# Kernel optimization log

Hardware: AMD Instinct MI355X
Metric: run time of the kernel (lower is better)

## Reference

```python
import jax, jax.numpy as jnp
import numpy as np

N_HEADS = 8
HEAD_DIM = 64


def setup_inputs() -> dict:
    key = jax.random.key(0)
    ks = jax.random.split(key, 5)
    B, L, D = 2, 2048, 512
    Dh = N_HEADS * HEAD_DIM  # 512
    scale_init = 0.02
    return {
        "x": jax.random.normal(ks[0], (B, L, D), dtype=jnp.float32),
        "wq": jax.random.normal(ks[1], (D, Dh), dtype=jnp.float32) * scale_init,
        "wk": jax.random.normal(ks[2], (D, Dh), dtype=jnp.float32) * scale_init,
        "wv": jax.random.normal(ks[3], (D, Dh), dtype=jnp.float32) * scale_init,
        "wo": jax.random.normal(ks[4], (Dh, D), dtype=jnp.float32) * scale_init,
    }


def reference(x, wq, wk, wv, wo):
    B, L, D = x.shape
    H, Dh = N_HEADS, HEAD_DIM
    scale = 1.0 / (Dh ** 0.5)

    q = (x @ wq).reshape(B, L, H, Dh)
    k = (x @ wk).reshape(B, L, H, Dh)
    v = (x @ wv).reshape(B, L, H, Dh)

    # [B, H, L, S] scores; diagonal (token attending to itself) is masked out.
    scores = jnp.einsum('blhe,bshe->bhls', q, k) * scale
    diag = jnp.eye(L, dtype=bool)  # [L, L]
    scores = jnp.where(diag, -jnp.inf, scores)
    attn = jax.nn.softmax(scores, axis=-1)

    out = jnp.einsum('bhls,bshd->blhd', attn, v).reshape(B, L, H * Dh)
    return out @ wo
```

## Files before the change

### kernel.cpp

```cpp
#include <hip/hip_runtime.h>
#include <hip/hip_bf16.h>
#include <math.h>

typedef __bf16 bf16;
typedef __bf16 bf16x8 __attribute__((ext_vector_type(8)));
typedef float f32x4 __attribute__((ext_vector_type(4)));
typedef unsigned int uint32x4 __attribute__((ext_vector_type(4)));

#define AS1 __attribute__((address_space(1)))
#define AS3 __attribute__((address_space(3)))

__device__ __forceinline__ void gload_lds16(const void* g, void* l) {
  __builtin_amdgcn_global_load_lds((const AS1 void*)g, (AS3 void*)l, 16, 0, 0);
}

__device__ __forceinline__ unsigned packbf16(float a, float b) {
  bf16 x = (bf16)a, y = (bf16)b;
  unsigned short ux, uy;
  __builtin_memcpy(&ux, &x, 2);
  __builtin_memcpy(&uy, &y, 2);
  return (unsigned)ux | ((unsigned)uy << 16);
}

__global__ __launch_bounds__(256) void cvt_x_kernel(const float* __restrict__ x,
                                                    bf16* __restrict__ xb) {
  int i = (blockIdx.x * 256 + threadIdx.x) * 8;
  float4 a = *(const float4*)(x + i);
  float4 b = *(const float4*)(x + i + 4);
  bf16x8 o;
  o[0] = (bf16)a.x; o[1] = (bf16)a.y; o[2] = (bf16)a.z; o[3] = (bf16)a.w;
  o[4] = (bf16)b.x; o[5] = (bf16)b.y; o[6] = (bf16)b.z; o[7] = (bf16)b.w;
  *(bf16x8*)(xb + i) = o;
}

__global__ __launch_bounds__(256) void transpose_w_kernel(
    const float* __restrict__ wq, const float* __restrict__ wk,
    const float* __restrict__ wv, const float* __restrict__ wo,
    bf16* __restrict__ wqkv_t, bf16* __restrict__ wo_t) {
  __shared__ float t[64 * 65];
  int ct = blockIdx.x & 31, kt = blockIdx.x >> 5;
  int p = ct >> 3;
  const float* src = (p == 0) ? wq : (p == 1) ? wk : (p == 2) ? wv : wo;
  int c0 = (ct & 7) * 64;
  int k0 = kt * 64;
  int tid = threadIdx.x;
  for (int i = 0; i < 16; ++i) {
    int idx = i * 256 + tid;
    int r = idx >> 6, c = idx & 63;
    t[r * 65 + c] = src[(size_t)(k0 + r) * 512 + c0 + c];
  }
  __syncthreads();
  for (int i = 0; i < 16; ++i) {
    int idx = i * 256 + tid;
    int cc = idx >> 6, kk = idx & 63;
    float v = t[kk * 65 + cc];
    int col = c0 + cc;
    if (p < 3) wqkv_t[(size_t)(p * 512 + col) * 512 + k0 + kk] = (bf16)v;
    else       wo_t[(size_t)col * 512 + k0 + kk] = (bf16)v;
  }
}

template <int MODE, int BM, int BN>
__global__ __launch_bounds__(256) void gemm_kernel(
    const bf16* __restrict__ A, const bf16* __restrict__ Bt,
    float* __restrict__ Cf, bf16* __restrict__ qw, bf16* __restrict__ kw,
    bf16* __restrict__ vtw, int M, int N, int K) {
  __shared__ bf16 ldsA[BM * 64];
  __shared__ bf16 ldsB[BN * 64];
  constexpr int MF = BM / 32;
  constexpr int NF = BN / 32;
  int tid = threadIdx.x;
  int wave = tid >> 6, l = tid & 63;
  int lr = l & 15, lg = l >> 4;
  int nbm = M / BM;
  int bm = blockIdx.x % nbm, bn = blockIdx.x / nbm;
  int wr = wave >> 1, wc = wave & 1;

  f32x4 acc[MF][NF] = {};

  for (int k0 = 0; k0 < K; k0 += 64) {
    #pragma unroll
    for (int i = 0; i < BM * 128 / 4096; ++i) {
      int off = i * 4096 + tid * 16;
      int r = off >> 7, cb = off & 127;
      gload_lds16((const char*)(A + (size_t)(bm * BM + r) * K + k0) + cb,
                  (char*)ldsA + i * 4096 + wave * 1024);
    }
    #pragma unroll
    for (int i = 0; i < BN * 128 / 4096; ++i) {
      int off = i * 4096 + tid * 16;
      int r = off >> 7, cb = off & 127;
      gload_lds16((const char*)(Bt + (size_t)(bn * BN + r) * K + k0) + cb,
                  (char*)ldsB + i * 4096 + wave * 1024);
    }
    __syncthreads();
    #pragma unroll
    for (int ks = 0; ks < 2; ++ks) {
      bf16x8 af[MF], bfr[NF];
      #pragma unroll
      for (int m = 0; m < MF; ++m)
        af[m] = *(const bf16x8*)(ldsA + (wr * (BM / 2) + m * 16 + lr) * 64 + ks * 32 + lg * 8);
      #pragma unroll
      for (int n = 0; n < NF; ++n)
        bfr[n] = *(const bf16x8*)(ldsB + (wc * (BN / 2) + n * 16 + lr) * 64 + ks * 32 + lg * 8);
      #pragma unroll
      for (int m = 0; m < MF; ++m)
        #pragma unroll
        for (int n = 0; n < NF; ++n)
          acc[m][n] = __builtin_amdgcn_mfma_f32_16x16x32_bf16(af[m], bfr[n], acc[m][n], 0, 0, 0);
    }
    __syncthreads();
  }

  #pragma unroll
  for (int m = 0; m < MF; ++m)
    #pragma unroll
    for (int n = 0; n < NF; ++n)
      #pragma unroll
      for (int j = 0; j < 4; ++j) {
        float v = acc[m][n][j];
        int row = bm * BM + wr * (BM / 2) + m * 16 + lg * 4 + j;
        int col = bn * BN + wc * (BN / 2) + n * 16 + lr;
        if (MODE == 1) {
          Cf[(size_t)row * N + col] = v;
        } else {
          int part = col >> 9, cp = col & 511;
          int h = cp >> 6, d = cp & 63;
          int b = row >> 11, lq = row & 2047;
          size_t bh = (size_t)(b * 8 + h);
          if (part == 0)      qw[(bh * 2048 + lq) * 64 + d] = (bf16)(v * 0.18033688f);
          else if (part == 1) kw[(bh * 2048 + lq) * 64 + d] = (bf16)v;
          else                vtw[(bh * 64 + d) * 2048 + lq] = (bf16)v;
        }
      }
}

__global__ __launch_bounds__(512, 4) void attn_kernel(
    const bf16* __restrict__ qw, const bf16* __restrict__ kw,
    const bf16* __restrict__ vtw,
    bf16* __restrict__ pO0, bf16* __restrict__ pO1,
    bf16* __restrict__ pO2, bf16* __restrict__ pO3,
    float* __restrict__ pL0, float* __restrict__ pL1,
    float* __restrict__ pL2, float* __restrict__ pL3) {
  __shared__ bf16 ldsK[2][64 * 64];
  __shared__ bf16 ldsV[2][64 * 64];

  int swzb = ((blockIdx.x & 7) << 6) | (blockIdx.x >> 3);
  int bh = swzb >> 5, qblk = (swzb >> 2) & 7, kv = swzb & 3;

  int tid = threadIdx.x, wave = tid >> 6, l = tid & 63;
  int lr = l & 15, lg = l >> 4;
  const bf16* Q  = qw  + (size_t)bh * 2048 * 64;
  const bf16* Kp = kw  + (size_t)bh * 2048 * 64;
  const bf16* Vt = vtw + (size_t)bh * 64 * 2048;
  int qbase = qblk * 256 + wave * 32;
  int td = qblk * 4 + (wave >> 1);
  int qoff = (wave & 1) * 32;

  bf16x8 qf[2][2];
  #pragma unroll
  for (int s = 0; s < 2; ++s)
    #pragma unroll
    for (int ks = 0; ks < 2; ++ks)
      qf[s][ks] = *(const bf16x8*)(Q + (size_t)(qbase + s * 16 + lr) * 64 + ks * 32 + lg * 8);

  int rowT = tid >> 3;
  int colT = (tid & 7) * 16;
  int swc = colT ^ ((((rowT & 3) | (((rowT >> 3) & 1) << 2))) << 4);

  int kxor = (((lr & 3) | (((lr >> 2) & 1) << 2)) << 4);
  int vxor = (((lr & 3) | (((lr >> 3) & 1) << 2)) << 4);

  f32x4 acc[2][4] = {};
  float lsum[2] = {0.f, 0.f};

  auto stage = [&](int buf, int t) {
    gload_lds16((const char*)Kp + (size_t)t * 8192 + rowT * 128 + swc,
                (char*)ldsK[buf] + wave * 1024);
    gload_lds16((const char*)Vt + (size_t)t * 128 + (size_t)rowT * 4096 + swc,
                (char*)ldsV[buf] + wave * 1024);
  };

  int t0 = kv * 8;
  stage(0, t0);

  for (int tt = 0; tt < 8; ++tt) {
    int t = t0 + tt;
    int buf = tt & 1;
    if (tt < 7) {
      stage(buf ^ 1, t + 1);
      asm volatile("s_waitcnt vmcnt(2)" ::: "memory");
    } else {
      asm volatile("s_waitcnt vmcnt(0)" ::: "memory");
    }
    __builtin_amdgcn_s_barrier();
    __builtin_amdgcn_sched_barrier(0);

    f32x4 ps[2][4] = {};
    __builtin_amdgcn_s_setprio(1);
    #pragma unroll
    for (int ks = 0; ks < 2; ++ks)
      #pragma unroll
      for (int n = 0; n < 4; ++n) {
        int mrow = ((n >> 1) << 5) + ((lr >> 2) << 3) + ((n & 1) << 2) + (lr & 3);
        bf16x8 kf = *(const bf16x8*)((const char*)ldsK[buf] + mrow * 128 +
                                     ((ks * 64 + lg * 16) ^ kxor));
        #pragma unroll
        for (int s = 0; s < 2; ++s)
          ps[s][n] = __builtin_amdgcn_mfma_f32_16x16x32_bf16(kf, qf[s][ks], ps[s][n], 0, 0, 0);
      }
    __builtin_amdgcn_s_setprio(0);

    if (t == td) {
      #pragma unroll
      for (int s = 0; s < 2; ++s)
        #pragma unroll
        for (int n = 0; n < 4; ++n)
          #pragma unroll
          for (int j = 0; j < 4; ++j)
            if (((n >> 1) * 32 + lg * 8 + (n & 1) * 4 + j) == qoff + s * 16 + lr)
              ps[s][n][j] = -INFINITY;
    }

    bf16x8 pf[2][2];
    #pragma unroll
    for (int s = 0; s < 2; ++s) {
      unsigned u[4][2];
      #pragma unroll
      for (int n = 0; n < 4; ++n) {
        float p0 = __builtin_amdgcn_exp2f(ps[s][n][0]);
        float p1 = __builtin_amdgcn_exp2f(ps[s][n][1]);
        float p2 = __builtin_amdgcn_exp2f(ps[s][n][2]);
        float p3 = __builtin_amdgcn_exp2f(ps[s][n][3]);
        lsum[s] += (p0 + p1) + (p2 + p3);
        u[n][0] = packbf16(p0, p1);
        u[n][1] = packbf16(p2, p3);
      }
      uint32x4 w0 = {u[0][0], u[0][1], u[1][0], u[1][1]};
      uint32x4 w1 = {u[2][0], u[2][1], u[3][0], u[3][1]};
      pf[s][0] = __builtin_bit_cast(bf16x8, w0);
      pf[s][1] = __builtin_bit_cast(bf16x8, w1);
    }

    __builtin_amdgcn_s_setprio(1);
    #pragma unroll
    for (int ks = 0; ks < 2; ++ks)
      #pragma unroll
      for (int n = 0; n < 4; ++n) {
        int vrow = n * 16 + lr;
        bf16x8 vf = *(const bf16x8*)((const char*)ldsV[buf] + vrow * 128 +
                                     ((ks * 64 + lg * 16) ^ vxor));
        #pragma unroll
        for (int s = 0; s < 2; ++s)
          acc[s][n] = __builtin_amdgcn_mfma_f32_16x16x32_bf16(pf[s][ks], vf, acc[s][n], 0, 0, 0);
      }
    __builtin_amdgcn_s_setprio(0);
    __builtin_amdgcn_s_barrier();
  }

  #pragma unroll
  for (int s = 0; s < 2; ++s) {
    lsum[s] += __shfl_xor(lsum[s], 16);
    lsum[s] += __shfl_xor(lsum[s], 32);
  }

  bf16*  pO = (kv == 0) ? pO0 : (kv == 1) ? pO1 : (kv == 2) ? pO2 : pO3;
  float* pL = (kv == 0) ? pL0 : (kv == 1) ? pL1 : (kv == 2) ? pL2 : pL3;
  #pragma unroll
  for (int s = 0; s < 2; ++s) {
    if (lg == 0) pL[(size_t)bh * 2048 + qbase + s * 16 + lr] = lsum[s];
    #pragma unroll
    for (int j = 0; j < 4; ++j) {
      int gq = qbase + s * 16 + lg * 4 + j;
      #pragma unroll
      for (int n = 0; n < 4; ++n)
        pO[((size_t)bh * 2048 + gq) * 64 + n * 16 + lr] = (bf16)acc[s][n][j];
    }
  }
}

__global__ __launch_bounds__(256) void combine_kernel(
    const bf16* __restrict__ pO0, const bf16* __restrict__ pO1,
    const bf16* __restrict__ pO2, const bf16* __restrict__ pO3,
    const float* __restrict__ pL0, const float* __restrict__ pL1,
    const float* __restrict__ pL2, const float* __restrict__ pL3,
    bf16* __restrict__ ao) {
  int idx = blockIdx.x * 256 + threadIdx.x;
  int e8 = idx * 8;
  int row = e8 >> 9, col = e8 & 511;
  int b = row >> 11, lq = row & 2047, h = col >> 6, d0 = col & 63;
  size_t bhq = (size_t)(b * 8 + h) * 2048 + lq;
  size_t src = bhq * 64 + d0;
  bf16x8 v0 = *(const bf16x8*)(pO0 + src);
  bf16x8 v1 = *(const bf16x8*)(pO1 + src);
  bf16x8 v2 = *(const bf16x8*)(pO2 + src);
  bf16x8 v3 = *(const bf16x8*)(pO3 + src);
  float inv = 1.f / (pL0[bhq] + pL1[bhq] + pL2[bhq] + pL3[bhq]);
  bf16x8 o;
  #pragma unroll
  for (int i = 0; i < 8; ++i)
    o[i] = (bf16)(((float)v0[i] + (float)v1[i] + (float)v2[i] + (float)v3[i]) * inv);
  *(bf16x8*)(ao + e8) = o;
}

extern "C" void kernel_launch(void* const* d_in, const int* in_sizes, int n_in,
                              void* d_out, int out_size, void* d_ws, size_t ws_size,
                              hipStream_t stream) {
  const float* x  = (const float*)d_in[0];
  const float* wq = (const float*)d_in[1];
  const float* wk = (const float*)d_in[2];
  const float* wv = (const float*)d_in[3];
  const float* wo = (const float*)d_in[4];

  if (ws_size < (32u << 20)) return;

  char* ws = (char*)d_ws;
  bf16* xb     = (bf16*)(ws);
  bf16* wqkv_t = (bf16*)(ws + (4 << 20));
  bf16* wo_t   = (bf16*)(ws + (6 << 20));
  bf16* q_ws   = (bf16*)(ws + (8 << 20));
  bf16* k_ws   = (bf16*)(ws + (12 << 20));
  bf16* vt_ws  = (bf16*)(ws + (16 << 20));
  bf16*  pO0 = (bf16*)(ws);
  float* pL0 = (float*)(ws + (4 << 20));
  float* pL1 = (float*)(ws + (4 << 20) + (128 << 10));
  float* pL2 = (float*)(ws + (4 << 20) + (256 << 10));
  float* pL3 = (float*)(ws + (4 << 20) + (384 << 10));
  bf16*  pO1 = (bf16*)(ws + (20 << 20));
  bf16*  pO2 = (bf16*)(ws + (24 << 20));
  bf16*  pO3 = (bf16*)(ws + (28 << 20));
  bf16*  ao  = (bf16*)(ws + (8 << 20));

  cvt_x_kernel<<<1024, 256, 0, stream>>>(x, xb);
  transpose_w_kernel<<<256, 256, 0, stream>>>(wq, wk, wv, wo, wqkv_t, wo_t);
  gemm_kernel<0, 64, 128><<<64 * 12, 256, 0, stream>>>(xb, wqkv_t, nullptr, q_ws, k_ws,
                                                       vt_ws, 4096, 1536, 512);
  attn_kernel<<<512, 512, 0, stream>>>(q_ws, k_ws, vt_ws, pO0, pO1, pO2, pO3,
                                       pL0, pL1, pL2, pL3);
  combine_kernel<<<1024, 256, 0, stream>>>(pO0, pO1, pO2, pO3, pL0, pL1, pL2, pL3, ao);
  gemm_kernel<1, 64, 64><<<64 * 8, 256, 0, stream>>>(ao, wo_t, (float*)d_out, nullptr,
                                                     nullptr, nullptr, 4096, 512, 512);
}
```

Measured before the change: 70.91 us.

## Fuse x conversion into QKV GEMM and load attention K/V directly from global

Drops the separate fp32-to-bf16 conversion kernel for x. The QKV GEMM now reads fp32 x, converts it in registers and stores bf16 to LDS, saving one launch and one round trip of x through memory. Separately, the attention kernel drops its double-buffered LDS staging of K and V, along with the swizzles and barriers, and each wave reads K/V fragments straight from global memory through the cache. This removes LDS traffic and synchronisation but loses the asynchronous prefetch and makes every wave fetch the shared K/V tiles on its own.

```diff
diff --git a/kernel.cpp b/kernel.cpp
--- a/kernel.cpp
+++ b/kernel.cpp
@@ -3,6 +3,7 @@
 #include <math.h>
 
 typedef __bf16 bf16;
+typedef __bf16 bf16x4 __attribute__((ext_vector_type(4)));
 typedef __bf16 bf16x8 __attribute__((ext_vector_type(8)));
 typedef float f32x4 __attribute__((ext_vector_type(4)));
 typedef unsigned int uint32x4 __attribute__((ext_vector_type(4)));
@@ -20,17 +21,6 @@
   __builtin_memcpy(&ux, &x, 2);
   __builtin_memcpy(&uy, &y, 2);
   return (unsigned)ux | ((unsigned)uy << 16);
-}
-
-__global__ __launch_bounds__(256) void cvt_x_kernel(const float* __restrict__ x,
-                                                    bf16* __restrict__ xb) {
-  int i = (blockIdx.x * 256 + threadIdx.x) * 8;
-  float4 a = *(const float4*)(x + i);
-  float4 b = *(const float4*)(x + i + 4);
-  bf16x8 o;
-  o[0] = (bf16)a.x; o[1] = (bf16)a.y; o[2] = (bf16)a.z; o[3] = (bf16)a.w;
-  o[4] = (bf16)b.x; o[5] = (bf16)b.y; o[6] = (bf16)b.z; o[7] = (bf16)b.w;
-  *(bf16x8*)(xb + i) = o;
 }
 
 __global__ __launch_bounds__(256) void transpose_w_kernel(
@@ -60,78 +50,126 @@
   }
 }
 
-template <int MODE, int BM, int BN>
-__global__ __launch_bounds__(256) void gemm_kernel(
-    const bf16* __restrict__ A, const bf16* __restrict__ Bt,
-    float* __restrict__ Cf, bf16* __restrict__ qw, bf16* __restrict__ kw,
-    bf16* __restrict__ vtw, int M, int N, int K) {
-  __shared__ bf16 ldsA[BM * 64];
-  __shared__ bf16 ldsB[BN * 64];
-  constexpr int MF = BM / 32;
-  constexpr int NF = BN / 32;
+__global__ __launch_bounds__(256) void gemm_qkv_kernel(
+    const float* __restrict__ x, const bf16* __restrict__ Bt,
+    bf16* __restrict__ qw, bf16* __restrict__ kw, bf16* __restrict__ vtw) {
+  __shared__ bf16 ldsA[64 * 64];
+  __shared__ bf16 ldsB[128 * 64];
   int tid = threadIdx.x;
   int wave = tid >> 6, l = tid & 63;
   int lr = l & 15, lg = l >> 4;
-  int nbm = M / BM;
+  int bm = blockIdx.x & 63, bn = blockIdx.x >> 6;
+  int wr = wave >> 1, wc = wave & 1;
+
+  f32x4 acc[2][4] = {};
+
+  for (int k0 = 0; k0 < 512; k0 += 64) {
+    #pragma unroll
+    for (int i = 0; i < 4; ++i) {
+      int off = i * 4096 + tid * 16;
+      int r = off >> 7, cb = off & 127;
+      gload_lds16((const char*)(Bt + (size_t)(bn * 128 + r) * 512 + k0) + cb,
+                  (char*)ldsB + i * 4096 + wave * 1024);
+    }
+    #pragma unroll
+    for (int c = 0; c < 4; ++c) {
+      int idx = c * 256 + tid;
+      int r = idx >> 4, f4 = idx & 15;
+      float4 v = *(const float4*)(x + (size_t)(bm * 64 + r) * 512 + k0 + f4 * 4);
+      bf16x4 o;
+      o[0] = (bf16)v.x; o[1] = (bf16)v.y; o[2] = (bf16)v.z; o[3] = (bf16)v.w;
+      *(bf16x4*)(ldsA + r * 64 + f4 * 4) = o;
+    }
+    __syncthreads();
+    #pragma unroll
+    for (int ks = 0; ks < 2; ++ks) {
+      bf16x8 af[2], bfr[4];
+      #pragma unroll
+      for (int m = 0; m < 2; ++m)
+        af[m] = *(const bf16x8*)(ldsA + (wr * 32 + m * 16 + lr) * 64 + ks * 32 + lg * 8);
+      #pragma unroll
+      for (int n = 0; n < 4; ++n)
+        bfr[n] = *(const bf16x8*)(ldsB + (wc * 64 + n * 16 + lr) * 64 + ks * 32 + lg * 8);
+      #pragma unroll
+      for (int m = 0; m < 2; ++m)
+        #pragma unroll
+        for (int n = 0; n < 4; ++n)
+          acc[m][n] = __builtin_amdgcn_mfma_f32_16x16x32_bf16(af[m], bfr[n], acc[m][n], 0, 0, 0);
+    }
+    __syncthreads();
+  }
+
+  #pragma unroll
+  for (int m = 0; m < 2; ++m)
+    #pragma unroll
+    for (int n = 0; n < 4; ++n)
+      #pragma unroll
+      for (int j = 0; j < 4; ++j) {
+        float v = acc[m][n][j];
+        int row = bm * 64 + wr * 32 + m * 16 + lg * 4 + j;
+        int col = bn * 128 + wc * 64 + n * 16 + lr;
+        int part = col >> 9, cp = col & 511;
+        int h = cp >> 6, d = cp & 63;
+        int b = row >> 11, lq = row & 2047;
+        size_t bh = (size_t)(b * 8 + h);
+        if (part == 0)      qw[(bh * 2048 + lq) * 64 + d] = (bf16)(v * 0.18033688f);
+        else if (part == 1) kw[(bh * 2048 + lq) * 64 + d] = (bf16)v;
+        else                vtw[(bh * 64 + d) * 2048 + lq] = (bf16)v;
+      }
+}
+
+__global__ __launch_bounds__(256) void gemm_out_kernel(
+    const bf16* __restrict__ A, const bf16* __restrict__ Bt,
+    float* __restrict__ Cf, int M, int N, int K) {
+  __shared__ bf16 ldsA[64 * 64];
+  __shared__ bf16 ldsB[64 * 64];
+  int tid = threadIdx.x;
+  int wave = tid >> 6, l = tid & 63;
+  int lr = l & 15, lg = l >> 4;
+  int nbm = M >> 6;
   int bm = blockIdx.x % nbm, bn = blockIdx.x / nbm;
   int wr = wave >> 1, wc = wave & 1;
 
-  f32x4 acc[MF][NF] = {};
+  f32x4 acc[2][2] = {};
 
   for (int k0 = 0; k0 < K; k0 += 64) {
     #pragma unroll
-    for (int i = 0; i < BM * 128 / 4096; ++i) {
+    for (int i = 0; i < 2; ++i) {
       int off = i * 4096 + tid * 16;
       int r = off >> 7, cb = off & 127;
-      gload_lds16((const char*)(A + (size_t)(bm * BM + r) * K + k0) + cb,
+      gload_lds16((const char*)(A + (size_t)(bm * 64 + r) * K + k0) + cb,
                   (char*)ldsA + i * 4096 + wave * 1024);
-    }
-    #pragma unroll
-    for (int i = 0; i < BN * 128 / 4096; ++i) {
-      int off = i * 4096 + tid * 16;
-      int r = off >> 7, cb = off & 127;
-      gload_lds16((const char*)(Bt + (size_t)(bn * BN + r) * K + k0) + cb,
+      gload_lds16((const char*)(Bt + (size_t)(bn * 64 + r) * K + k0) + cb,
                   (char*)ldsB + i * 4096 + wave * 1024);
     }
     __syncthreads();
     #pragma unroll
     for (int ks = 0; ks < 2; ++ks) {
-      bf16x8 af[MF], bfr[NF];
-      #pragma unroll
-      for (int m = 0; m < MF; ++m)
-        af[m] = *(const bf16x8*)(ldsA + (wr * (BM / 2) + m * 16 + lr) * 64 + ks * 32 + lg * 8);
-      #pragma unroll
-      for (int n = 0; n < NF; ++n)
-        bfr[n] = *(const bf16x8*)(ldsB + (wc * (BN / 2) + n * 16 + lr) * 64 + ks * 32 + lg * 8);
-      #pragma unroll
-      for (int m = 0; m < MF; ++m)
-        #pragma unroll
-        for (int n = 0; n < NF; ++n)
+      bf16x8 af[2], bfr[2];
+      #pragma unroll
+      for (int m = 0; m < 2; ++m)
+        af[m] = *(const bf16x8*)(ldsA + (wr * 32 + m * 16 + lr) * 64 + ks * 32 + lg * 8);
+      #pragma unroll
+      for (int n = 0; n < 2; ++n)
+        bfr[n] = *(const bf16x8*)(ldsB + (wc * 32 + n * 16 + lr) * 64 + ks * 32 + lg * 8);
+      #pragma unroll
+      for (int m = 0; m < 2; ++m)
+        #pragma unroll
+        for (int n = 0; n < 2; ++n)
           acc[m][n] = __builtin_amdgcn_mfma_f32_16x16x32_bf16(af[m], bfr[n], acc[m][n], 0, 0, 0);
     }
     __syncthreads();
   }
 
   #pragma unroll
-  for (int m = 0; m < MF; ++m)
-    #pragma unroll
-    for (int n = 0; n < NF; ++n)
+  for (int m = 0; m < 2; ++m)
+    #pragma unroll
+    for (int n = 0; n < 2; ++n)
       #pragma unroll
       for (int j = 0; j < 4; ++j) {
-        float v = acc[m][n][j];
-        int row = bm * BM + wr * (BM / 2) + m * 16 + lg * 4 + j;
-        int col = bn * BN + wc * (BN / 2) + n * 16 + lr;
-        if (MODE == 1) {
-          Cf[(size_t)row * N + col] = v;
-        } else {
-          int part = col >> 9, cp = col & 511;
-          int h = cp >> 6, d = cp & 63;
-          int b = row >> 11, lq = row & 2047;
-          size_t bh = (size_t)(b * 8 + h);
-          if (part == 0)      qw[(bh * 2048 + lq) * 64 + d] = (bf16)(v * 0.18033688f);
-          else if (part == 1) kw[(bh * 2048 + lq) * 64 + d] = (bf16)v;
-          else                vtw[(bh * 64 + d) * 2048 + lq] = (bf16)v;
-        }
+        int row = bm * 64 + wr * 32 + m * 16 + lg * 4 + j;
+        int col = bn * 64 + wc * 32 + n * 16 + lr;
+        Cf[(size_t)row * N + col] = acc[m][n][j];
       }
 }
 
@@ -142,17 +180,14 @@
     bf16* __restrict__ pO2, bf16* __restrict__ pO3,
     float* __restrict__ pL0, float* __restrict__ pL1,
     float* __restrict__ pL2, float* __restrict__ pL3) {
-  __shared__ bf16 ldsK[2][64 * 64];
-  __shared__ bf16 ldsV[2][64 * 64];
-
   int swzb = ((blockIdx.x & 7) << 6) | (blockIdx.x >> 3);
   int bh = swzb >> 5, qblk = (swzb >> 2) & 7, kv = swzb & 3;
 
   int tid = threadIdx.x, wave = tid >> 6, l = tid & 63;
   int lr = l & 15, lg = l >> 4;
   const bf16* Q  = qw  + (size_t)bh * 2048 * 64;
-  const bf16* Kp = kw  + (size_t)bh * 2048 * 64;
-  const bf16* Vt = vtw + (size_t)bh * 64 * 2048;
+  const char* Kb = (const char*)(kw  + (size_t)bh * 2048 * 64);
+  const char* Vb = (const char*)(vtw + (size_t)bh * 64 * 2048);
   int qbase = qblk * 256 + wave * 32;
   int td = qblk * 4 + (wave >> 1);
   int qoff = (wave & 1) * 32;
@@ -164,37 +199,15 @@
     for (int ks = 0; ks < 2; ++ks)
       qf[s][ks] = *(const bf16x8*)(Q + (size_t)(qbase + s * 16 + lr) * 64 + ks * 32 + lg * 8);
 
-  int rowT = tid >> 3;
-  int colT = (tid & 7) * 16;
-  int swc = colT ^ ((((rowT & 3) | (((rowT >> 3) & 1) << 2))) << 4);
-
-  int kxor = (((lr & 3) | (((lr >> 2) & 1) << 2)) << 4);
-  int vxor = (((lr & 3) | (((lr >> 3) & 1) << 2)) << 4);
+  int mbase = ((lr >> 2) << 3) + (lr & 3);
+  int cb = lg * 16;
 
   f32x4 acc[2][4] = {};
   float lsum[2] = {0.f, 0.f};
 
-  auto stage = [&](int buf, int t) {
-    gload_lds16((const char*)Kp + (size_t)t * 8192 + rowT * 128 + swc,
-                (char*)ldsK[buf] + wave * 1024);
-    gload_lds16((const char*)Vt + (size_t)t * 128 + (size_t)rowT * 4096 + swc,
-                (char*)ldsV[buf] + wave * 1024);
-  };
-
   int t0 = kv * 8;
-  stage(0, t0);
-
   for (int tt = 0; tt < 8; ++tt) {
     int t = t0 + tt;
-    int buf = tt & 1;
-    if (tt < 7) {
-      stage(buf ^ 1, t + 1);
-      asm volatile("s_waitcnt vmcnt(2)" ::: "memory");
-    } else {
-      asm volatile("s_waitcnt vmcnt(0)" ::: "memory");
-    }
-    __builtin_amdgcn_s_barrier();
-    __builtin_amdgcn_sched_barrier(0);
 
     f32x4 ps[2][4] = {};
     __builtin_amdgcn_s_setprio(1);
@@ -202,9 +215,8 @@
     for (int ks = 0; ks < 2; ++ks)
       #pragma unroll
       for (int n = 0; n < 4; ++n) {
-        int mrow = ((n >> 1) << 5) + ((lr >> 2) << 3) + ((n & 1) << 2) + (lr & 3);
-        bf16x8 kf = *(const bf16x8*)((const char*)ldsK[buf] + mrow * 128 +
-                                     ((ks * 64 + lg * 16) ^ kxor));
+        int mrow = ((n >> 1) << 5) + ((n & 1) << 2) + mbase;
+        bf16x8 kf = *(const bf16x8*)(Kb + (size_t)t * 8192 + mrow * 128 + ks * 64 + cb);
         #pragma unroll
         for (int s = 0; s < 2; ++s)
           ps[s][n] = __builtin_amdgcn_mfma_f32_16x16x32_bf16(kf, qf[s][ks], ps[s][n], 0, 0, 0);
@@ -247,15 +259,12 @@
     for (int ks = 0; ks < 2; ++ks)
       #pragma unroll
       for (int n = 0; n < 4; ++n) {
-        int vrow = n * 16 + lr;
-        bf16x8 vf = *(const bf16x8*)((const char*)ldsV[buf] + vrow * 128 +
-                                     ((ks * 64 + lg * 16) ^ vxor));
+        bf16x8 vf = *(const bf16x8*)(Vb + (size_t)(n * 16 + lr) * 4096 + t * 128 + ks * 64 + cb);
         #pragma unroll
         for (int s = 0; s < 2; ++s)
           acc[s][n] = __builtin_amdgcn_mfma_f32_16x16x32_bf16(pf[s][ks], vf, acc[s][n], 0, 0, 0);
       }
     __builtin_amdgcn_s_setprio(0);
-    __builtin_amdgcn_s_barrier();
   }
 
   #pragma unroll
@@ -315,7 +324,6 @@
   if (ws_size < (32u << 20)) return;
 
   char* ws = (char*)d_ws;
-  bf16* xb     = (bf16*)(ws);
   bf16* wqkv_t = (bf16*)(ws + (4 << 20));
   bf16* wo_t   = (bf16*)(ws + (6 << 20));
   bf16* q_ws   = (bf16*)(ws + (8 << 20));
@@ -331,13 +339,10 @@
   bf16*  pO3 = (bf16*)(ws + (28 << 20));
   bf16*  ao  = (bf16*)(ws + (8 << 20));
 
-  cvt_x_kernel<<<1024, 256, 0, stream>>>(x, xb);
   transpose_w_kernel<<<256, 256, 0, stream>>>(wq, wk, wv, wo, wqkv_t, wo_t);
-  gemm_kernel<0, 64, 128><<<64 * 12, 256, 0, stream>>>(xb, wqkv_t, nullptr, q_ws, k_ws,
-                                                       vt_ws, 4096, 1536, 512);
+  gemm_qkv_kernel<<<64 * 12, 256, 0, stream>>>(x, wqkv_t, q_ws, k_ws, vt_ws);
   attn_kernel<<<512, 512, 0, stream>>>(q_ws, k_ws, vt_ws, pO0, pO1, pO2, pO3,
                                        pL0, pL1, pL2, pL3);
   combine_kernel<<<1024, 256, 0, stream>>>(pO0, pO1, pO2, pO3, pL0, pL1, pL2, pL3, ao);
-  gemm_kernel<1, 64, 64><<<64 * 8, 256, 0, stream>>>(ao, wo_t, (float*)d_out, nullptr,
-                                                     nullptr, nullptr, 4096, 512, 512);
-}
+  gemm_out_kernel<<<64 * 8, 256, 0, stream>>>(ao, wo_t, (float*)d_out, 4096, 512, 512);
+}
```

Measured after the change: 107.9 us. +52.1%, slower.
